# Kernel tuning notes

Hardware: AMD Instinct MI355X
Metric: run time of the kernel (lower is better)

The kernel has to match this reference:

```python
import jax, jax.numpy as jnp
import numpy as np

V, E, H = 32000, 512, 1024  # vocab, embed_dim, hidden_dim
B, S = 32, 64
PAD = 0


def _init(key, shape, fan_in):
    return jax.random.normal(key, shape, jnp.float32) * (1.0 / np.sqrt(fan_in))


def setup_inputs() -> dict:
    key = jax.random.key(0)
    ks = jax.random.split(key, 16)
    tok_embed = _init(ks[0], (V, E), E).at[PAD].set(0.0)  # padding_idx row zeroed
    inp = {
        "image_emb": jax.random.normal(ks[1], (B, E), jnp.float32),
        "retrieved_emb": jax.random.normal(ks[2], (B, E), jnp.float32),
        "tokens_in": jax.random.randint(ks[3], (B, S), 0, V, jnp.int64),
        "tok_embed": tok_embed,
        "init_h_W": _init(ks[4], (H, E), E),
        "init_h_b": jnp.zeros((H,), jnp.float32),
        "gru_W_ih": _init(ks[5], (3 * H, 2 * E), 2 * E),
        "gru_W_hh": _init(ks[6], (3 * H, H), H),
        "gru_b_ih": jnp.zeros((3 * H,), jnp.float32),
        "gru_b_hh": jnp.zeros((3 * H,), jnp.float32),
        "gate_W": _init(ks[7], (1, H + 2 * E), H + 2 * E),
        "gate_b": jnp.zeros((1,), jnp.float32),
        "out_W": _init(ks[8], (V, H), H),
        "out_b": jnp.zeros((V,), jnp.float32),
    }
    return inp


def _gru_cell(x, h, W_ih, W_hh, b_ih, b_hh):
    # PyTorch GRU cell math
    gi = x @ W_ih.T + b_ih  # [B, 3H]
    gh = h @ W_hh.T + b_hh
    i_r, i_z, i_n = jnp.split(gi, 3, axis=-1)
    h_r, h_z, h_n = jnp.split(gh, 3, axis=-1)
    r = jax.nn.sigmoid(i_r + h_r)
    z = jax.nn.sigmoid(i_z + h_z)
    n = jnp.tanh(i_n + r * h_n)
    return (1.0 - z) * n + z * h


def reference(image_emb, retrieved_emb, tokens_in, tok_embed, init_h_W, init_h_b,
              gru_W_ih, gru_W_hh, gru_b_ih, gru_b_hh, gate_W, gate_b, out_W, out_b):
    tok = tok_embed[tokens_in]  # [B, S, E]
    h0 = jnp.tanh(image_emb @ init_h_W.T + init_h_b)  # [B, H]

    def step(h, x_t):
        gate_in = jnp.concatenate([h, image_emb, retrieved_emb], axis=-1)  # [B, H+2E]
        alpha = jax.nn.sigmoid(gate_in @ gate_W.T + gate_b)  # [B, 1]
        fused = alpha * image_emb + (1.0 - alpha) * retrieved_emb  # [B, E]
        gru_in = jnp.concatenate([x_t, fused], axis=-1)  # [B, 2E]
        h_new = _gru_cell(gru_in, h, gru_W_ih, gru_W_hh, gru_b_ih, gru_b_hh)
        logit = h_new @ out_W.T + out_b  # [B, V]
        return h_new, logit

    _, logits = jax.lax.scan(step, h0, jnp.swapaxes(tok, 0, 1))  # [S, B, V]
    return jnp.swapaxes(logits, 0, 1)  # [B, S, V]
```

## Files before the change

kernel.cpp:

```cpp
#include <hip/hip_runtime.h>
#include <hip/hip_bf16.h>
#include <stdint.h>

#define B_ 32
#define S_ 64
#define E_ 512
#define H_ 1024
#define V_ 32000
#define H3_ 3072
#define NPROD 64
#define NCONS 192
#define NGRID (NPROD + NCONS)
#define NPANEL 250
#define NGROUP 8
#define NJOBS (NPANEL * NGROUP)

typedef __bf16 bf16x8 __attribute__((ext_vector_type(8)));
typedef float f32x4 __attribute__((ext_vector_type(4)));
using bf16 = __hip_bfloat16;

__device__ __forceinline__ unsigned short f2bf(float f) {
  __hip_bfloat16 h = __float2bfloat16(f);
  return __builtin_bit_cast(unsigned short, h);
}
__device__ __forceinline__ float bf2f(unsigned short u) {
  return __bfloat162float(__builtin_bit_cast(__hip_bfloat16, u));
}

__device__ __forceinline__ void async16(void* lds, const void* g) {
  __builtin_amdgcn_global_load_lds(
      (const __attribute__((address_space(1))) unsigned int*)g,
      (__attribute__((address_space(3))) unsigned int*)lds, 16, 0, 0);
}

__device__ __forceinline__ void st_u32(unsigned* p, unsigned v) {
  __hip_atomic_store(p, v, __ATOMIC_RELAXED, __HIP_MEMORY_SCOPE_AGENT);
}
__device__ __forceinline__ unsigned ld_u32(const unsigned* p) {
  return __hip_atomic_load(p, __ATOMIC_RELAXED, __HIP_MEMORY_SCOPE_AGENT);
}

__device__ __forceinline__ int hswz(int b, int ig) {
  return ((((b >> 4) * 32 + (ig >> 5)) * 64) + ((b & 15) + (((ig >> 3) & 3) << 4))) * 8 + (ig & 7);
}


__global__ void gather_tok(const int* __restrict__ toks, const float* __restrict__ emb,
                           bf16* __restrict__ Abf) {
  int m = blockIdx.x;
  int b = m & 31, t = m >> 5;
  int token = toks[b * S_ + t];
  const float* src = emb + (size_t)token * E_;
  bf16* dst = Abf + (size_t)m * E_;
  int k = threadIdx.x * 4;
  f32x4 v = *(const f32x4*)(src + k);
  dst[k + 0] = __float2bfloat16(v[0]);
  dst[k + 1] = __float2bfloat16(v[1]);
  dst[k + 2] = __float2bfloat16(v[2]);
  dst[k + 3] = __float2bfloat16(v[3]);
}

__global__ void cvt_wihx(const float* __restrict__ Wih, bf16* __restrict__ Wx) {
  int j = blockIdx.x;
  int k = threadIdx.x * 4;
  f32x4 v = *(const f32x4*)(Wih + (size_t)j * 1024 + k);
  bf16* d = Wx + (size_t)j * 512 + k;
  d[0] = __float2bfloat16(v[0]);
  d[1] = __float2bfloat16(v[1]);
  d[2] = __float2bfloat16(v[2]);
  d[3] = __float2bfloat16(v[3]);
}

__global__ __launch_bounds__(256) void prep_kernel(
    const bf16* __restrict__ Abf, const bf16* __restrict__ Wihx, float* __restrict__ gix,
    const float* __restrict__ img, const float* __restrict__ retr,
    const float* __restrict__ ihW, const float* __restrict__ ihb,
    const float* __restrict__ Wih, const float* __restrict__ gW,
    const float* __restrict__ gb, const float* __restrict__ outW,
    ushort* __restrict__ Wb, float* __restrict__ h32, bf16* __restrict__ hbf0,
    float* __restrict__ u, float* __restrict__ v, float* __restrict__ cg) {
  __shared__ __align__(16) char psm[66048];
  int bid = blockIdx.x, tid = threadIdx.x;

  if (bid < 384) {
    const int nb = 384, mtiles = 16;
    bf16* Ald = (bf16*)psm;
    bf16* Bld = (bf16*)(psm + 8192);
    int swz = (bid & 7) * (nb >> 3) + (bid >> 3);
    int tm = swz % mtiles, tn = swz / mtiles;
    int l = tid & 63, w = tid >> 6;
    const int K = 512, N = H3_;
    const bf16* ga = Abf + (size_t)(tm * 128 + w * 16 + (l >> 2)) * K + (l & 3) * 8;
    const bf16* gbp = Wihx + (size_t)(tn * 128 + w * 16 + (l >> 2)) * K + (l & 3) * 8;
    char* lA = (char*)Ald + w * 1024;
    char* lB = (char*)Bld + w * 1024;
    f32x4 acc[4][4] = {};
    int wm = (w >> 1) * 64, wn = (w & 1) * 64;
    int lr = l & 15, lk = (l >> 4) * 8;
    for (int kt = 0; kt < K; kt += 32) {
      async16(lA, ga);
      async16(lA + 4096, ga + (size_t)64 * K);
      async16(lB, gbp);
      async16(lB + 4096, gbp + (size_t)64 * K);
      ga += 32; gbp += 32;
      __syncthreads();
      bf16x8 af[4], bfv[4];
#pragma unroll
      for (int mi = 0; mi < 4; ++mi) af[mi] = *(const bf16x8*)&Ald[(wm + mi * 16 + lr) * 32 + lk];
#pragma unroll
      for (int ni = 0; ni < 4; ++ni) bfv[ni] = *(const bf16x8*)&Bld[(wn + ni * 16 + lr) * 32 + lk];
#pragma unroll
      for (int mi = 0; mi < 4; ++mi)
#pragma unroll
        for (int ni = 0; ni < 4; ++ni)
          acc[mi][ni] = __builtin_amdgcn_mfma_f32_16x16x32_bf16(af[mi], bfv[ni], acc[mi][ni], 0, 0, 0);
      __syncthreads();
    }
    int cr = (l >> 4) * 4, cc = l & 15;
#pragma unroll
    for (int mi = 0; mi < 4; ++mi)
#pragma unroll
      for (int ni = 0; ni < 4; ++ni) {
        int col = tn * 128 + wn + ni * 16 + cc;
#pragma unroll
        for (int rr = 0; rr < 4; ++rr) {
          int row = tm * 128 + wm + mi * 16 + cr + rr;
          gix[(size_t)row * N + col] = acc[mi][ni][rr];
        }
      }

  } else if (bid < 1152) {
    int local = bid - 384;
    bool isU = local < 384;
    const float* src = isU ? img : retr;
    float* dst = isU ? u : v;
    int j0 = (isU ? local : local - 384) * 8;
    float(*sim)[E_ + 1] = (float(*)[E_ + 1])psm;
    for (int i = tid; i < B_ * E_ / 4; i += 256) {
      f32x4 vv = ((const f32x4*)src)[i];
      int r = (i * 4) / E_, c = (i * 4) % E_;
      sim[r][c + 0] = vv[0]; sim[r][c + 1] = vv[1]; sim[r][c + 2] = vv[2]; sim[r][c + 3] = vv[3];
    }
    __syncthreads();
    int b = tid & 31;
    int j = j0 + (tid >> 5);
    const float* wr = Wih + (size_t)j * 1024 + 512;
    float acc = 0.f;
    for (int k = 0; k < E_; k += 4) {
      f32x4 w4 = *(const f32x4*)(wr + k);
      acc += w4[0] * sim[b][k] + w4[1] * sim[b][k + 1] + w4[2] * sim[b][k + 2] + w4[3] * sim[b][k + 3];
    }
    dst[b * H3_ + j] = acc;

  } else if (bid < 1280) {
    int local = bid - 1152;
    float(*sim)[E_ + 1] = (float(*)[E_ + 1])psm;
    for (int i = tid; i < B_ * E_ / 4; i += 256) {
      f32x4 vv = ((const f32x4*)img)[i];
      int r = (i * 4) / E_, c = (i * 4) % E_;
      sim[r][c + 0] = vv[0]; sim[r][c + 1] = vv[1]; sim[r][c + 2] = vv[2]; sim[r][c + 3] = vv[3];
    }
    __syncthreads();
    int b = tid & 31, il = tid >> 5;
    int i = local * 8 + il;
    const float* wr = ihW + (size_t)i * E_;
    float acc = 0.f;
    for (int k = 0; k < E_; k += 4) {
      f32x4 w4 = *(const f32x4*)(wr + k);
      acc += w4[0] * sim[b][k] + w4[1] * sim[b][k + 1] + w4[2] * sim[b][k + 2] + w4[3] * sim[b][k + 3];
    }
    float hv = tanhf(acc + ihb[i]);
    h32[b * H_ + i] = hv;
    hbf0[hswz(b, i)] = __float2bfloat16(hv);

  } else if (bid < 1312) {
    int b = bid - 1280;
    float* red = (float*)psm;
    float acc = 0.f;
    for (int k = tid; k < E_; k += 256)
      acc += img[b * E_ + k] * gW[1024 + k] + retr[b * E_ + k] * gW[1536 + k];
    red[tid] = acc;
    __syncthreads();
    for (int s = 128; s > 0; s >>= 1) {
      if (tid < s) red[tid] += red[tid + s];
      __syncthreads();
    }
    if (tid == 0) cg[b] = red[0] + gb[0];

  } else {
    long n4 = (long)V_ * H_ / 4;
    long stride = 1024L * 256;
    for (long i = (long)(bid - 1312) * 256 + tid; i < n4; i += stride) {
      f32x4 vv = *(const f32x4*)(outW + i * 4);
      ushort4 o;
      o.x = f2bf(vv[0]); o.y = f2bf(vv[1]); o.z = f2bf(vv[2]); o.w = f2bf(vv[3]);
      ((ushort4*)Wb)[i] = o;
    }
  }
}

__device__ __forceinline__ void step_sync(unsigned* flags, int bi, unsigned val) {
  __syncthreads();
  if (threadIdx.x == 0) st_u32(flags + bi * 32, val);
  if (threadIdx.x < NPROD) {
    const unsigned* f = flags + threadIdx.x * 32;
    while (ld_u32(f) < val) __builtin_amdgcn_s_sleep(1);
  }
  __syncthreads();
}

__global__ __launch_bounds__(256, 1) void fused_persist(
    const float* __restrict__ Whh, const float* __restrict__ gixAll,
    const float* __restrict__ u, const float* __restrict__ v,
    const float* __restrict__ cg, const float* __restrict__ gW,
    const float* __restrict__ bih, const float* __restrict__ bhh,
    const float* __restrict__ h32init, bf16* __restrict__ hbf,
    unsigned* __restrict__ flags, const bf16* __restrict__ Wb,
    const float* __restrict__ outb, float* __restrict__ out) {
  __shared__ __align__(16) char smem[32768];
  int bi = blockIdx.x;
  int tid = threadIdx.x;

  if (bi < NPROD) {
    int w = tid >> 6, l = tid & 63;
    int lr = l & 15, lk8 = (l >> 4) * 8;
    int kbase = w * 256;
    float(*red)[4][2][64][4] = (float(*)[4][2][64][4])smem;

    bf16x8 whi[3][8], wlo[3][8];
#pragma unroll
    for (int g = 0; g < 3; ++g)
#pragma unroll
      for (int ks = 0; ks < 8; ++ks) {
        const float* wp = Whh + (size_t)(g * H_ + bi * 16 + lr) * H_ + kbase + ks * 32 + lk8;
        f32x4 a0 = *(const f32x4*)wp;
        f32x4 a1 = *(const f32x4*)(wp + 4);
        bf16x8 h8, l8;
#pragma unroll
        for (int jj = 0; jj < 4; ++jj) {
          unsigned short hb0 = f2bf(a0[jj]);
          unsigned short hb1 = f2bf(a1[jj]);
          h8[jj] = __builtin_bit_cast(__bf16, hb0);
          h8[jj + 4] = __builtin_bit_cast(__bf16, hb1);
          l8[jj] = __builtin_bit_cast(__bf16, f2bf(a0[jj] - bf2f(hb0)));
          l8[jj + 4] = __builtin_bit_cast(__bf16, f2bf(a1[jj] - bf2f(hb1)));
        }
        whi[g][ks] = h8;
        wlo[g][ks] = l8;
      }
    bf16x8 gwf[8];
#pragma unroll
    for (int ks = 0; ks < 8; ++ks) {
      int kk = (w * 8 + ks) * 32 + (l >> 4) * 8;
      f32x4 g0 = *(const f32x4*)(gW + kk);
      f32x4 g1 = *(const f32x4*)(gW + kk + 4);
      bf16x8 gf;
#pragma unroll
      for (int jj = 0; jj < 4; ++jj) {
        gf[jj] = __builtin_bit_cast(__bf16, f2bf(g0[jj]));
        gf[jj + 4] = __builtin_bit_cast(__bf16, f2bf(g1[jj]));
      }
      gwf[ks] = gf;
    }

    int bq = tid >> 3;
    int il0 = (tid & 7) * 2;
    float uq[2][3], vq[2][3], biq[2][3], bhq[2][3], hold[2];
    float cgq = cg[bq];
#pragma unroll
    for (int q = 0; q < 2; ++q) {
      int ig = bi * 16 + il0 + q;
#pragma unroll
      for (int g = 0; g < 3; ++g) {
        uq[q][g] = u[bq * H3_ + g * H_ + ig];
        vq[q][g] = v[bq * H3_ + g * H_ + ig];
        biq[q][g] = bih[g * H_ + ig];
        bhq[q][g] = bhh[g * H_ + ig];
      }
      hold[q] = h32init[bq * H_ + ig];
    }
    int btq = bq >> 4, breg = bq & 3, lrow = ((bq & 15) >> 2) * 16;

    float gxn[2][3];
    {
      const float* gx = gixAll + (size_t)bq * H3_;
#pragma unroll
      for (int q = 0; q < 2; ++q) {
        int ig = bi * 16 + il0 + q;
        gxn[q][0] = gx[ig];
        gxn[q][1] = gx[H_ + ig];
        gxn[q][2] = gx[2 * H_ + ig];
      }
    }

    for (int t = 0; t < S_; ++t) {
      const f32x4* hb4 = (const f32x4*)((const char*)hbf + (size_t)t * 65536);
      bf16x8 hh_all[2][8];
#pragma unroll
      for (int bt = 0; bt < 2; ++bt)
#pragma unroll
        for (int ks = 0; ks < 8; ++ks)
          hh_all[bt][ks] = __builtin_bit_cast(bf16x8, hb4[(bt * 32 + w * 8 + ks) * 64 + l]);
      float gxv[2][3];
#pragma unroll
      for (int q = 0; q < 2; ++q) {
        gxv[q][0] = gxn[q][0]; gxv[q][1] = gxn[q][1]; gxv[q][2] = gxn[q][2];
      }
      asm volatile("s_waitcnt vmcnt(0)" ::: "memory");
      __builtin_amdgcn_sched_barrier(0);

      f32x4 acc[4][2] = {};
#pragma unroll
      for (int ks = 0; ks < 8; ++ks) {
#pragma unroll
        for (int bt = 0; bt < 2; ++bt) {
          bf16x8 hh = hh_all[bt][ks];
          acc[0][bt] = __builtin_amdgcn_mfma_f32_16x16x32_bf16(hh, whi[0][ks], acc[0][bt], 0, 0, 0);
          acc[0][bt] = __builtin_amdgcn_mfma_f32_16x16x32_bf16(hh, wlo[0][ks], acc[0][bt], 0, 0, 0);
          acc[1][bt] = __builtin_amdgcn_mfma_f32_16x16x32_bf16(hh, whi[1][ks], acc[1][bt], 0, 0, 0);
          acc[1][bt] = __builtin_amdgcn_mfma_f32_16x16x32_bf16(hh, wlo[1][ks], acc[1][bt], 0, 0, 0);
          acc[2][bt] = __builtin_amdgcn_mfma_f32_16x16x32_bf16(hh, whi[2][ks], acc[2][bt], 0, 0, 0);
          acc[2][bt] = __builtin_amdgcn_mfma_f32_16x16x32_bf16(hh, wlo[2][ks], acc[2][bt], 0, 0, 0);
          acc[3][bt] = __builtin_amdgcn_mfma_f32_16x16x32_bf16(hh, gwf[ks], acc[3][bt], 0, 0, 0);
        }
      }
#pragma unroll
      for (int g = 0; g < 4; ++g)
#pragma unroll
        for (int bt = 0; bt < 2; ++bt)
          *(f32x4*)&red[w][g][bt][l][0] = acc[g][bt];
      __syncthreads();

      int lane0 = lrow + il0;
      float ad = red[0][3][btq][lane0][breg] + red[1][3][btq][lane0][breg] +
                 red[2][3][btq][lane0][breg] + red[3][3][btq][lane0][breg];
      float a = 1.f / (1.f + expf(-(ad + cgq)));
      unsigned short h16[2];
#pragma unroll
      for (int q = 0; q < 2; ++q) {
        int lane = lrow + il0 + q;
        float sr = red[0][0][btq][lane][breg] + red[1][0][btq][lane][breg] +
                   red[2][0][btq][lane][breg] + red[3][0][btq][lane][breg];
        float sz = red[0][1][btq][lane][breg] + red[1][1][btq][lane][breg] +
                   red[2][1][btq][lane][breg] + red[3][1][btq][lane][breg];
        float sn = red[0][2][btq][lane][breg] + red[1][2][btq][lane][breg] +
                   red[2][2][btq][lane][breg] + red[3][2][btq][lane][breg];
        float ir = gxv[q][0] + a * uq[q][0] + (1.f - a) * vq[q][0] + biq[q][0];
        float iz = gxv[q][1] + a * uq[q][1] + (1.f - a) * vq[q][1] + biq[q][1];
        float in_ = gxv[q][2] + a * uq[q][2] + (1.f - a) * vq[q][2] + biq[q][2];
        float r = 1.f / (1.f + expf(-(ir + sr + bhq[q][0])));
        float z = 1.f / (1.f + expf(-(iz + sz + bhq[q][1])));
        float nn = tanhf(in_ + r * (sn + bhq[q][2]));
        float hv = (1.f - z) * nn + z * hold[q];
        hold[q] = hv;
        h16[q] = f2bf(hv);
      }
      {
        unsigned hipack = (unsigned)h16[0] | ((unsigned)h16[1] << 16);
        int off = hswz(bq, bi * 16 + il0);
        unsigned* hi32 = (unsigned*)hbf + (size_t)(t + 1) * 16384;
        st_u32(hi32 + (off >> 1), hipack);
      }
      if (t < S_ - 1) {
        const float* gx = gixAll + ((size_t)(t + 1) * B_ + bq) * H3_;
#pragma unroll
        for (int q = 0; q < 2; ++q) {
          int ig = bi * 16 + il0 + q;
          gxn[q][0] = gx[ig];
          gxn[q][1] = gx[H_ + ig];
          gxn[q][2] = gx[2 * H_ + ig];
        }
        step_sync(flags, bi, t + 1);
      }
    }
    __syncthreads();
    if (tid == 0) st_u32(flags + bi * 32, S_);

  } else {
    int c = bi - NPROD;
    int l = tid & 63, w = tid >> 6;
    int wm = (w >> 1) * 64, wn = (w & 1) * 64;
    int lr = l & 15, lk = (l >> 4) * 8;
    bf16* Bld = (bf16*)smem;
    const char* hb_base = (const char*)hbf;

    for (int j = c; j < NJOBS; j += NCONS) {
      int group = j / NPANEL;
      int panel = j - group * NPANEL;
      int s0 = group * 8 + 1;
      unsigned need = (unsigned)(group * 8 + 8);
      if (w == 0) {
        const unsigned* f = flags + l * 32;
        while (ld_u32(f) < need) __builtin_amdgcn_s_sleep(16);
      }
      __builtin_amdgcn_sched_barrier(0);
      __builtin_amdgcn_s_barrier();
      __builtin_amdgcn_sched_barrier(0);

      const bf16* gb = Wb + (size_t)(panel * 128 + w * 16 + (l >> 2)) * 1024 + (l & 3) * 8;
      f32x4 acc[2][4][4] = {};
      bf16x8 afr[2][2][4];
#pragma unroll
      for (int mt = 0; mt < 2; ++mt)
#pragma unroll
        for (int mi = 0; mi < 4; ++mi) {
          int r16 = mt * 8 + (wm >> 4) + mi;
          const f32x4* pa = (const f32x4*)(hb_base + (size_t)(s0 + (r16 >> 1)) * 65536 +
                                           (((r16 & 1) * 32 + 0) * 64 + l) * 16);
          afr[0][mt][mi] = __builtin_bit_cast(bf16x8, *pa);
        }
#pragma unroll
      for (int kt = 0; kt < 32; ++kt) {
        char* lB = smem + (kt & 1) * 8192 + w * 1024;
        async16(lB, gb);
        async16(lB + 4096, gb + (size_t)64 * 1024);
        gb += 32;
        if (kt < 31) {
#pragma unroll
          for (int mt = 0; mt < 2; ++mt)
#pragma unroll
            for (int mi = 0; mi < 4; ++mi) {
              int r16 = mt * 8 + (wm >> 4) + mi;
              const f32x4* pa = (const f32x4*)(hb_base + (size_t)(s0 + (r16 >> 1)) * 65536 +
                                               (((r16 & 1) * 32 + (kt + 1)) * 64 + l) * 16);
              afr[(kt + 1) & 1][mt][mi] = __builtin_bit_cast(bf16x8, *pa);
            }
          asm volatile("s_waitcnt vmcnt(8)" ::: "memory");
        } else {
          asm volatile("s_waitcnt vmcnt(0)" ::: "memory");
        }
        __builtin_amdgcn_sched_barrier(0);
        __builtin_amdgcn_s_barrier();
        __builtin_amdgcn_sched_barrier(0);
        const bf16* Bh = Bld + (kt & 1) * 4096;
        bf16x8 bfv[4];
#pragma unroll
        for (int ni = 0; ni < 4; ++ni)
          bfv[ni] = *(const bf16x8*)&Bh[(wn + ni * 16 + lr) * 32 + lk];
#pragma unroll
        for (int mt = 0; mt < 2; ++mt)
#pragma unroll
          for (int mi = 0; mi < 4; ++mi)
#pragma unroll
            for (int ni = 0; ni < 4; ++ni)
              acc[mt][mi][ni] = __builtin_amdgcn_mfma_f32_16x16x32_bf16(afr[kt & 1][mt][mi], bfv[ni],
                                                                        acc[mt][mi][ni], 0, 0, 0);
      }
      int cr = (l >> 4) * 4, cc = l & 15;
#pragma unroll
      for (int mt = 0; mt < 2; ++mt)
#pragma unroll
        for (int mi = 0; mi < 4; ++mi)
#pragma unroll
          for (int ni = 0; ni < 4; ++ni) {
            int col = panel * 128 + wn + ni * 16 + cc;
            float bv = outb[col];
#pragma unroll
            for (int rr = 0; rr < 4; ++rr) {
              int gr = mt * 128 + wm + mi * 16 + cr + rr;
              int t = group * 8 + (gr >> 5);
              int b = gr & 31;
              out[(size_t)(b * S_ + t) * V_ + col] = acc[mt][mi][ni][rr] + bv;
            }
          }
    }
  }
}

extern "C" void kernel_launch(void* const* d_in, const int* in_sizes, int n_in, void* d_out,
                              int out_size, void* d_ws, size_t ws_size, hipStream_t stream) {
  const float* img  = (const float*)d_in[0];
  const float* retr = (const float*)d_in[1];
  const int*   toks = (const int*)d_in[2];
  const float* temb = (const float*)d_in[3];
  const float* ihW  = (const float*)d_in[4];
  const float* ihb  = (const float*)d_in[5];
  const float* Wih  = (const float*)d_in[6];
  const float* Whh  = (const float*)d_in[7];
  const float* bih  = (const float*)d_in[8];
  const float* bhh  = (const float*)d_in[9];
  const float* gW   = (const float*)d_in[10];
  const float* gb   = (const float*)d_in[11];
  const float* outW = (const float*)d_in[12];
  const float* outb = (const float*)d_in[13];
  float* out = (float*)d_out;

  char* ws = (char*)d_ws;
  bf16* Wb     = (bf16*)ws;  ws += (size_t)V_ * H_ * 2;
  float* gix   = (float*)ws; ws += (size_t)S_ * B_ * H3_ * 4;
  bf16* Wihx   = (bf16*)ws;  ws += (size_t)H3_ * E_ * 2;
  bf16* Abf    = (bf16*)ws;  ws += (size_t)B_ * S_ * E_ * 2;
  float* u     = (float*)ws; ws += (size_t)B_ * H3_ * 4;
  float* v     = (float*)ws; ws += (size_t)B_ * H3_ * 4;
  float* h32i  = (float*)ws; ws += (size_t)B_ * H_ * 4;
  bf16* hbf    = (bf16*)ws;  ws += (size_t)(S_ + 1) * B_ * H_ * 2;
  float* cg    = (float*)ws; ws += 128;
  unsigned* flags = (unsigned*)ws; ws += NPROD * 32 * 4;

  gather_tok<<<B_ * S_, 128, 0, stream>>>(toks, temb, Abf);
  cvt_wihx<<<H3_, 128, 0, stream>>>(Wih, Wihx);
  (void)hipMemsetAsync(flags, 0, NPROD * 32 * 4, stream);

  prep_kernel<<<2336, 256, 0, stream>>>(Abf, Wihx, gix, img, retr, ihW, ihb, Wih, gW, gb,
                                        outW, (ushort*)Wb, h32i, hbf, u, v, cg);

  fused_persist<<<NGRID, 256, 0, stream>>>(Whh, gix, u, v, cg, gW, bih, bhh, h32i,
                                           hbf, flags, Wb, outb, out);
}
```

Before: 403.2 us.

## Overlap output-weight bf16 conversion with recurrence in consumer blocks; merge prep kernels

Moves the fp32-to-bf16 conversion of the 32000x1024 output weight out of prep_kernel and into the consumer blocks of the persistent kernel. There it runs while producer blocks work through the GRU recurrence, and a cross-block flag barrier among the consumers guards it. The gather and Wih conversion kernels are also merged into one launch to remove a launch. The intent is to hide the large conversion pass behind the serial recurrence and shorten the prep critical path. The cost is a new inter-block spin barrier, plus memory bandwidth contention with the producers.

```diff
diff --git a/kernel.cpp b/kernel.cpp
--- a/kernel.cpp
+++ b/kernel.cpp
@@ -44,31 +44,30 @@
   return ((((b >> 4) * 32 + (ig >> 5)) * 64) + ((b & 15) + (((ig >> 3) & 3) << 4))) * 8 + (ig & 7);
 }
 
-
-__global__ void gather_tok(const int* __restrict__ toks, const float* __restrict__ emb,
-                           bf16* __restrict__ Abf) {
-  int m = blockIdx.x;
-  int b = m & 31, t = m >> 5;
-  int token = toks[b * S_ + t];
-  const float* src = emb + (size_t)token * E_;
-  bf16* dst = Abf + (size_t)m * E_;
+__global__ void feed_kernel(const int* __restrict__ toks, const float* __restrict__ emb,
+                            bf16* __restrict__ Abf, const float* __restrict__ Wih,
+                            bf16* __restrict__ Wx) {
+  int bid = blockIdx.x;
   int k = threadIdx.x * 4;
-  f32x4 v = *(const f32x4*)(src + k);
-  dst[k + 0] = __float2bfloat16(v[0]);
-  dst[k + 1] = __float2bfloat16(v[1]);
-  dst[k + 2] = __float2bfloat16(v[2]);
-  dst[k + 3] = __float2bfloat16(v[3]);
-}
-
-__global__ void cvt_wihx(const float* __restrict__ Wih, bf16* __restrict__ Wx) {
-  int j = blockIdx.x;
-  int k = threadIdx.x * 4;
-  f32x4 v = *(const f32x4*)(Wih + (size_t)j * 1024 + k);
-  bf16* d = Wx + (size_t)j * 512 + k;
-  d[0] = __float2bfloat16(v[0]);
-  d[1] = __float2bfloat16(v[1]);
-  d[2] = __float2bfloat16(v[2]);
-  d[3] = __float2bfloat16(v[3]);
+  if (bid < B_ * S_) {
+    int b = bid & 31, t = bid >> 5;
+    int token = toks[b * S_ + t];
+    const float* src = emb + (size_t)token * E_;
+    bf16* dst = Abf + (size_t)bid * E_;
+    f32x4 v = *(const f32x4*)(src + k);
+    dst[k + 0] = __float2bfloat16(v[0]);
+    dst[k + 1] = __float2bfloat16(v[1]);
+    dst[k + 2] = __float2bfloat16(v[2]);
+    dst[k + 3] = __float2bfloat16(v[3]);
+  } else {
+    int j = bid - B_ * S_;
+    f32x4 v = *(const f32x4*)(Wih + (size_t)j * 1024 + k);
+    bf16* d = Wx + (size_t)j * 512 + k;
+    d[0] = __float2bfloat16(v[0]);
+    d[1] = __float2bfloat16(v[1]);
+    d[2] = __float2bfloat16(v[2]);
+    d[3] = __float2bfloat16(v[3]);
+  }
 }
 
 __global__ __launch_bounds__(256) void prep_kernel(
@@ -76,8 +75,7 @@
     const float* __restrict__ img, const float* __restrict__ retr,
     const float* __restrict__ ihW, const float* __restrict__ ihb,
     const float* __restrict__ Wih, const float* __restrict__ gW,
-    const float* __restrict__ gb, const float* __restrict__ outW,
-    ushort* __restrict__ Wb, float* __restrict__ h32, bf16* __restrict__ hbf0,
+    const float* __restrict__ gb, float* __restrict__ h32, bf16* __restrict__ hbf0,
     float* __restrict__ u, float* __restrict__ v, float* __restrict__ cg) {
   __shared__ __align__(16) char psm[66048];
   int bid = blockIdx.x, tid = threadIdx.x;
@@ -173,7 +171,7 @@
     h32[b * H_ + i] = hv;
     hbf0[hswz(b, i)] = __float2bfloat16(hv);
 
-  } else if (bid < 1312) {
+  } else {
     int b = bid - 1280;
     float* red = (float*)psm;
     float acc = 0.f;
@@ -186,16 +184,6 @@
       __syncthreads();
     }
     if (tid == 0) cg[b] = red[0] + gb[0];
-
-  } else {
-    long n4 = (long)V_ * H_ / 4;
-    long stride = 1024L * 256;
-    for (long i = (long)(bid - 1312) * 256 + tid; i < n4; i += stride) {
-      f32x4 vv = *(const f32x4*)(outW + i * 4);
-      ushort4 o;
-      o.x = f2bf(vv[0]); o.y = f2bf(vv[1]); o.z = f2bf(vv[2]); o.w = f2bf(vv[3]);
-      ((ushort4*)Wb)[i] = o;
-    }
   }
 }
 
@@ -215,7 +203,8 @@
     const float* __restrict__ cg, const float* __restrict__ gW,
     const float* __restrict__ bih, const float* __restrict__ bhh,
     const float* __restrict__ h32init, bf16* __restrict__ hbf,
-    unsigned* __restrict__ flags, const bf16* __restrict__ Wb,
+    unsigned* __restrict__ flags, unsigned* __restrict__ cflags,
+    const float* __restrict__ outW, bf16* __restrict__ Wb,
     const float* __restrict__ outb, float* __restrict__ out) {
   __shared__ __align__(16) char smem[32768];
   int bi = blockIdx.x;
@@ -384,6 +373,26 @@
     bf16* Bld = (bf16*)smem;
     const char* hb_base = (const char*)hbf;
 
+    for (int p = c; p < NPANEL; p += NCONS) {
+      const float* srcp = outW + (size_t)p * 131072;
+      ushort* dstp = (ushort*)Wb + (size_t)p * 131072;
+      for (int i = tid; i < 32768; i += 256) {
+        f32x4 v4 = *(const f32x4*)(srcp + (size_t)i * 4);
+        ushort4 o;
+        o.x = f2bf(v4[0]); o.y = f2bf(v4[1]); o.z = f2bf(v4[2]); o.w = f2bf(v4[3]);
+        ((ushort4*)dstp)[i] = o;
+      }
+    }
+    __syncthreads();
+    __builtin_amdgcn_fence(__ATOMIC_RELEASE, "agent");
+    if (tid == 0) st_u32(cflags + c * 32, 1);
+    if (tid < NCONS) {
+      const unsigned* f = cflags + tid * 32;
+      while (ld_u32(f) < 1) __builtin_amdgcn_s_sleep(16);
+    }
+    __syncthreads();
+    __builtin_amdgcn_fence(__ATOMIC_ACQUIRE, "agent");
+
     for (int j = c; j < NJOBS; j += NCONS) {
       int group = j / NPANEL;
       int panel = j - group * NPANEL;
@@ -495,15 +504,15 @@
   float* h32i  = (float*)ws; ws += (size_t)B_ * H_ * 4;
   bf16* hbf    = (bf16*)ws;  ws += (size_t)(S_ + 1) * B_ * H_ * 2;
   float* cg    = (float*)ws; ws += 128;
-  unsigned* flags = (unsigned*)ws; ws += NPROD * 32 * 4;
-
-  gather_tok<<<B_ * S_, 128, 0, stream>>>(toks, temb, Abf);
-  cvt_wihx<<<H3_, 128, 0, stream>>>(Wih, Wihx);
-  (void)hipMemsetAsync(flags, 0, NPROD * 32 * 4, stream);
-
-  prep_kernel<<<2336, 256, 0, stream>>>(Abf, Wihx, gix, img, retr, ihW, ihb, Wih, gW, gb,
-                                        outW, (ushort*)Wb, h32i, hbf, u, v, cg);
+  unsigned* flags  = (unsigned*)ws; ws += NPROD * 32 * 4;
+  unsigned* cflags = (unsigned*)ws; ws += NCONS * 32 * 4;
+
+  feed_kernel<<<B_ * S_ + H3_, 128, 0, stream>>>(toks, temb, Abf, Wih, Wihx);
+  (void)hipMemsetAsync(flags, 0, (NPROD + NCONS) * 32 * 4, stream);
+
+  prep_kernel<<<1312, 256, 0, stream>>>(Abf, Wihx, gix, img, retr, ihW, ihb, Wih, gW, gb,
+                                        h32i, hbf, u, v, cg);
 
   fused_persist<<<NGRID, 256, 0, stream>>>(Whh, gix, u, v, cg, gW, bih, bhh, h32i,
-                                           hbf, flags, Wb, outb, out);
-}
+                                           hbf, flags, cflags, outW, Wb, outb, out);
+}
```

New measurement: 461.2 us. +14.4%, slower.
